# Kernel tuning notes

Measured on AMD Instinct MI355X. Metric: run time of the kernel, lower is better.

Reference implementation:

```python
import jax, jax.numpy as jnp
import numpy as np


def setup_inputs() -> dict:
    key = jax.random.key(0)
    k1, k2 = jax.random.split(key)
    x = jax.random.normal(k1, (1, 48, 56, 56), dtype=jnp.float32)
    w = jax.random.normal(k2, (24, 96, 7), dtype=jnp.float32)
    return {"x": x, "w": w, "shift": 1}


def reference(x, w, shift):
    # The torch unfold + einsum is a grouped cross-correlation along W:
    #   x viewed as (1, groups=2, Cin=24, H=56, W=56)
    #   out[l,o,k,n,m] = sum_{i,j} x[l,o,i,n, m+j-3] * w[i,k,j]   (zero-padded)
    # Same weight w is shared by both groups -> duplicate it per group.
    wt = jnp.transpose(w, (1, 0, 2))               # (96, 24, 7)  OIK per group
    kernel = jnp.concatenate([wt, wt], axis=0)     # (192, 24, 7) both groups
    kernel = kernel[:, :, None, :]                 # (O=192, I=24, KH=1, KW=7)
    y = jax.lax.conv_general_dilated(
        x, kernel,
        window_strides=(1, 1),
        padding=((0, 0), (3, 3)),                  # 'same' along W only
        dimension_numbers=("NCHW", "OIHW", "NCHW"),
        feature_group_count=2,
    )                                              # (1, 192, 56, 56)
    # torch.roll(t, shift, dims=2): roll along H
    return jnp.roll(y, shift, axis=2)
```

## Files before the change

### kernel.cpp

```cpp
#include <hip/hip_runtime.h>


#define H 56
#define W 56
#define C_GRP 24
#define KW 7
#define HW (H * W)

__global__ __launch_bounds__(64) void conv7_roll_kernel(
    const float* __restrict__ x,
    const float* __restrict__ w,
    const int* __restrict__ shift_p,
    float* __restrict__ out)
{
    const int o     = blockIdx.x;
    const int htile = blockIdx.y;
    const int lane  = threadIdx.x;
    const int r     = lane >> 3;
    const int s     = lane & 7;
    const int h_out = htile * 8 + r;
    const int wbase = s * 7;

    const int g  = o / 96;
    const int oc = o % 96;

    __shared__ float wl[C_GRP * KW];
    for (int t = lane; t < C_GRP * KW; t += 64) {
        const int i = t / 7;
        const int k = t - i * 7;
        wl[t] = w[i * (96 * 7) + oc * 7 + k];
    }
    __syncthreads();

    const int shift = shift_p[0];
    int hi = (h_out - shift) % H;
    if (hi < 0) hi += H;

    float acc[7] = {0.f, 0.f, 0.f, 0.f, 0.f, 0.f, 0.f};

    const float* xg = x + (g * C_GRP) * HW + hi * W;

    for (int i = 0; i < C_GRP; ++i) {
        const float* xr = xg + i * HW;
        float xv[13];
        #pragma unroll
        for (int j = 0; j < 13; ++j) {
            const int p = wbase - 3 + j;
            xv[j] = (p >= 0 && p < W) ? xr[p] : 0.0f;
        }
        #pragma unroll
        for (int k = 0; k < KW; ++k) {
            const float wk = wl[i * KW + k];
            #pragma unroll
            for (int j = 0; j < 7; ++j)
                acc[j] += xv[j + k] * wk;
        }
    }

    float* op = out + o * HW + h_out * W + wbase;
    #pragma unroll
    for (int j = 0; j < 7; ++j)
        op[j] = acc[j];
}

extern "C" void kernel_launch(void* const* d_in, const int* in_sizes, int n_in,
                              void* d_out, int out_size, void* d_ws, size_t ws_size,
                              hipStream_t stream)
{
    const float* x     = (const float*)d_in[0];
    const float* w     = (const float*)d_in[1];
    const int*   shift = (const int*)d_in[2];
    float*       out   = (float*)d_out;

    dim3 grid(192, 7);
    conv7_roll_kernel<<<grid, 64, 0, stream>>>(x, w, shift, out);
}
```

Measured before the change: 71.96 us.

## Vectorize conv with float4 loads and share input rows across output channels

Each thread now computes 4 contiguous outputs for 2 output channels, loading the input row as three aligned float4 vectors (left, center, right) instead of 13 scalar guarded loads. A block handles 4 output channels over 4 rows with 128 threads, and weights are padded to 8 per row in shared memory so they can be read as float4. The intent is to cut redundant global input loads and scalar memory instructions and to get vectorized stores. In exchange, 2 of every 16 lanes do redundant work, and the grid has fewer, larger blocks.

```diff
diff --git a/kernel.cpp b/kernel.cpp
--- a/kernel.cpp
+++ b/kernel.cpp
@@ -1,66 +1,90 @@
 #include <hip/hip_runtime.h>
 
 
-#define H 56
-#define W 56
-#define C_GRP 24
+#define Hh 56
+#define Wd 56
+#define HWsz (Hh * Wd)
+#define CI 24
 #define KW 7
-#define HW (H * W)
+#define OCB 4
 
-__global__ __launch_bounds__(64) void conv7_roll_kernel(
+__global__ __launch_bounds__(128) void conv7_roll_kernel(
     const float* __restrict__ x,
     const float* __restrict__ w,
     const int* __restrict__ shift_p,
     float* __restrict__ out)
 {
-    const int o     = blockIdx.x;
-    const int htile = blockIdx.y;
-    const int lane  = threadIdx.x;
-    const int r     = lane >> 3;
-    const int s     = lane & 7;
-    const int h_out = htile * 8 + r;
-    const int wbase = s * 7;
+    const int tid  = threadIdx.x;
+    const int wid  = tid >> 6;
+    const int lane = tid & 63;
+    const int rl   = lane >> 4;
+    const int c4r  = lane & 15;
+    const int c4   = c4r < 13 ? c4r : 13;
 
-    const int g  = o / 96;
-    const int oc = o % 96;
+    const int obase = blockIdx.x * OCB;
+    const int g     = obase / 96;
+    const int ocb96 = obase - g * 96;
 
-    __shared__ float wl[C_GRP * KW];
-    for (int t = lane; t < C_GRP * KW; t += 64) {
-        const int i = t / 7;
-        const int k = t - i * 7;
-        wl[t] = w[i * (96 * 7) + oc * 7 + k];
+    __shared__ __align__(16) float wl[OCB * CI * 8];
+    for (int t = tid; t < OCB * CI * 8; t += 128) {
+        const int oc_l = t / (CI * 8);
+        const int rem  = t - oc_l * (CI * 8);
+        const int ci   = rem >> 3;
+        const int k    = rem & 7;
+        wl[t] = (k < KW) ? w[ci * (96 * KW) + (ocb96 + oc_l) * KW + k] : 0.0f;
     }
     __syncthreads();
 
     const int shift = shift_p[0];
-    int hi = (h_out - shift) % H;
-    if (hi < 0) hi += H;
+    const int h_out = blockIdx.y * 4 + rl;
+    int hi = (h_out - shift) % Hh;
+    if (hi < 0) hi += Hh;
 
-    float acc[7] = {0.f, 0.f, 0.f, 0.f, 0.f, 0.f, 0.f};
+    const float* xp = x + g * (CI * HWsz) + hi * Wd + c4 * 4;
+    const float* lp = xp + (c4 > 0  ? -4 : 0);
+    const float* rp = xp + (c4 < 13 ?  4 : 0);
+    const bool lz = (c4 == 0);
+    const bool rz = (c4 >= 13);
 
-    const float* xg = x + (g * C_GRP) * HW + hi * W;
+    const float* wl0 = &wl[(wid * 2    ) * (CI * 8)];
+    const float* wl1 = &wl[(wid * 2 + 1) * (CI * 8)];
 
-    for (int i = 0; i < C_GRP; ++i) {
-        const float* xr = xg + i * HW;
-        float xv[13];
-        #pragma unroll
-        for (int j = 0; j < 13; ++j) {
-            const int p = wbase - 3 + j;
-            xv[j] = (p >= 0 && p < W) ? xr[p] : 0.0f;
-        }
+    float a0[4] = {0.f, 0.f, 0.f, 0.f};
+    float a1[4] = {0.f, 0.f, 0.f, 0.f};
+
+    #pragma unroll 4
+    for (int ci = 0; ci < CI; ++ci) {
+        float4 M = *(const float4*)(xp + ci * HWsz);
+        float4 L = *(const float4*)(lp + ci * HWsz);
+        float4 R = *(const float4*)(rp + ci * HWsz);
+        if (lz) { L.x = 0.f; L.y = 0.f; L.z = 0.f; L.w = 0.f; }
+        if (rz) { R.x = 0.f; R.y = 0.f; R.z = 0.f; R.w = 0.f; }
+        float xv[12] = {L.x, L.y, L.z, L.w, M.x, M.y, M.z, M.w, R.x, R.y, R.z, R.w};
+
+        float4 wa = *(const float4*)(wl0 + ci * 8);
+        float4 wb = *(const float4*)(wl0 + ci * 8 + 4);
+        float4 wc = *(const float4*)(wl1 + ci * 8);
+        float4 wd = *(const float4*)(wl1 + ci * 8 + 4);
+        float w0[7] = {wa.x, wa.y, wa.z, wa.w, wb.x, wb.y, wb.z};
+        float w1[7] = {wc.x, wc.y, wc.z, wc.w, wd.x, wd.y, wd.z};
+
         #pragma unroll
         for (int k = 0; k < KW; ++k) {
-            const float wk = wl[i * KW + k];
             #pragma unroll
-            for (int j = 0; j < 7; ++j)
-                acc[j] += xv[j + k] * wk;
+            for (int j = 0; j < 4; ++j) {
+                a0[j] += xv[1 + j + k] * w0[k];
+                a1[j] += xv[1 + j + k] * w1[k];
+            }
         }
     }
 
-    float* op = out + o * HW + h_out * W + wbase;
-    #pragma unroll
-    for (int j = 0; j < 7; ++j)
-        op[j] = acc[j];
+    if (c4r < 14) {
+        const int o0 = obase + wid * 2;
+        float* op0 = out + o0 * HWsz + h_out * Wd + c4 * 4;
+        float* op1 = op0 + HWsz;
+        *(float4*)op0 = make_float4(a0[0], a0[1], a0[2], a0[3]);
+        *(float4*)op1 = make_float4(a1[0], a1[1], a1[2], a1[3]);
+    }
 }
 
 extern "C" void kernel_launch(void* const* d_in, const int* in_sizes, int n_in,
@@ -72,6 +96,6 @@
     const int*   shift = (const int*)d_in[2];
     float*       out   = (float*)d_out;
 
-    dim3 grid(192, 7);
-    conv7_roll_kernel<<<grid, 64, 0, stream>>>(x, w, shift, out);
+    dim3 grid(48, 14);
+    conv7_roll_kernel<<<grid, 128, 0, stream>>>(x, w, shift, out);
 }
```

New measurement: 68.66 us. 1.05x faster.
